# Performance work log

Hardware: AMD Instinct MI355X
Metric: run time of the kernel (lower is better)

The kernel has to match this reference:

```python
import jax, jax.numpy as jnp
import numpy as np

EMBED_DIM = 2048
NUM_HEADS = 16
HEAD_DIM = EMBED_DIM // NUM_HEADS
LATENT_DIM = 512


def setup_inputs() -> dict:
    key = jax.random.key(0)
    ks = jax.random.split(key, 6)
    s = 1.0 / np.sqrt(EMBED_DIM)
    sl = 1.0 / np.sqrt(LATENT_DIM)
    x = jax.random.normal(ks[0], (2, 2048, EMBED_DIM), dtype=jnp.float32)
    # nn.Linear stores weight as [out, in]; we keep [in, out] for x @ W
    W_q = jax.random.uniform(ks[1], (EMBED_DIM, EMBED_DIM), jnp.float32, -s, s)
    W_c = jax.random.uniform(ks[2], (EMBED_DIM, LATENT_DIM), jnp.float32, -s, s)
    W_k = jax.random.uniform(ks[3], (LATENT_DIM, EMBED_DIM), jnp.float32, -sl, sl)
    W_v = jax.random.uniform(ks[4], (LATENT_DIM, EMBED_DIM), jnp.float32, -sl, sl)
    W_o = jax.random.uniform(ks[5], (EMBED_DIM, EMBED_DIM), jnp.float32, -s, s)
    return {"x": x, "W_q": W_q, "W_c": W_c, "W_k": W_k, "W_v": W_v, "W_o": W_o}


def reference(x, W_q, W_c, W_k, W_v, W_o):
    B, S, _ = x.shape
    H, D = NUM_HEADS, HEAD_DIM
    Q = (x @ W_q).reshape(B, S, H, D)          # [B,S,H,D]
    C = x @ W_c                                 # [B,S,latent]
    K = (C @ W_k).reshape(B, S, H, D)
    V = (C @ W_v).reshape(B, S, H, D)
    scale = 1.0 / np.sqrt(D).astype(np.float32)
    scores = jnp.einsum('bqhd,bkhd->bhqk', Q, K) * scale
    probs = jax.nn.softmax(scores, axis=-1)
    attn = jnp.einsum('bhqk,bkhd->bqhd', probs, V).reshape(B, S, H * D)
    return attn @ W_o
```

## Files before the change

kernel.cpp:

```cpp
#include <hip/hip_runtime.h>
#include <hip/hip_bf16.h>
#include <cstdint>
#include <cstddef>

#define EDIM 2048
#define SLEN 2048
#define BATCH 2
#define NH 16
#define HD 128
#define LAT 512
#define MROWS (BATCH * SLEN)

#define QPREMUL (0.08838834764831845f * 1.44269504088896340f)

typedef __bf16 bf16;
typedef __bf16 bf16x8 __attribute__((ext_vector_type(8)));
typedef __bf16 bf16x4 __attribute__((ext_vector_type(4)));
typedef float f32x4 __attribute__((ext_vector_type(4)));
typedef float f32x16 __attribute__((ext_vector_type(16)));

#define AS1 __attribute__((address_space(1)))
#define AS3 __attribute__((address_space(3)))

__device__ __forceinline__ void gload_lds16(const void* g, void* l) {
  __builtin_amdgcn_global_load_lds((const AS1 void*)g, (AS3 void*)l, 16, 0, 0);
}

__global__ __launch_bounds__(256) void cvt_f32_bf16(const float* __restrict__ in,
                                                    bf16* __restrict__ out, int n4) {
  int i = blockIdx.x * blockDim.x + threadIdx.x;
  int stride = gridDim.x * blockDim.x;
  for (; i < n4; i += stride) {
    float4 v = reinterpret_cast<const float4*>(in)[i];
    bf16x4 o = {(bf16)v.x, (bf16)v.y, (bf16)v.z, (bf16)v.w};
    reinterpret_cast<bf16x4*>(out)[i] = o;
  }
}

__global__ __launch_bounds__(256) void transpose_cvt(const float* __restrict__ W,
                                                     bf16* __restrict__ Wt,
                                                     int K, int N) {
  __shared__ float tile[32][33];
  const int tx = threadIdx.x, ty = threadIdx.y;
  const int n0 = blockIdx.x * 32, k0 = blockIdx.y * 32;
#pragma unroll
  for (int i = 0; i < 4; ++i)
    tile[ty + i * 8][tx] = W[(size_t)(k0 + ty + i * 8) * N + n0 + tx];
  __syncthreads();
#pragma unroll
  for (int i = 0; i < 4; ++i)
    Wt[(size_t)(n0 + ty + i * 8) * K + k0 + tx] = (bf16)tile[tx][ty + i * 8];
}

enum { P_F32 = 0, P_QC = 1, P_FRAGKV = 2 };

#define BUFSZ 24576

#define STAGE_B_UNIT(dstbuf, k0)                                                 \
  {                                                                              \
    _Pragma("unroll") for (int jj = 0; jj < 2; ++jj) {                           \
      int L = t + jj * 512;                                                      \
      int row = L >> 3, c = L & 7;                                               \
      gload_lds16(Bt + (size_t)(n0 + row) * K + (k0) + ((c ^ (row & 7)) << 3),   \
                  (dstbuf) + 16384 + L * 8);                                     \
    }                                                                            \
  }

#define STAGE_A_PART(dstbuf, k0, jj)                                             \
  {                                                                              \
    int L = t256 + (jj) * 256;                                                   \
    int row = ahalf * 128 + (L >> 3), c = L & 7;                                 \
    gload_lds16(A + (size_t)(m0 + row) * K + (k0) + ((c ^ (row & 7)) << 3),      \
                (dstbuf) + row * 64 + c * 8);                                    \
  }

template <int MODE>
__global__ __launch_bounds__(512, 1)
void gemm8p(const bf16* __restrict__ A, const bf16* __restrict__ Bt,
            float* __restrict__ Cf, bf16* __restrict__ Cb, bf16* __restrict__ Cb2,
            int M, int N, int K) {
  extern __shared__ bf16 lds[];
  const int t = threadIdx.x;
  const int wid = t >> 6, l = t & 63, lo = l & 15, hi = l >> 4;
  const int wr = wid >> 1, wc = wid & 1;
  const int lin = blockIdx.y * gridDim.x + blockIdx.x;
  const int cpx = (gridDim.x * gridDim.y) >> 3;
  const int sw = (lin & 7) * cpx + (lin >> 3);
  const int m0 = (sw / gridDim.x) * 256, n0 = (sw % gridDim.x) * 128;
  const int nk = K >> 6;
  const int t256 = t & 255, ahalf = t >> 8;

  int aoff[2][4], boff[2][4];
#pragma unroll
  for (int kk = 0; kk < 2; ++kk)
#pragma unroll
    for (int m = 0; m < 4; ++m) {
      int ra = wr * 64 + m * 16 + lo;
      aoff[kk][m] = ra * 64 + (((kk * 4 + hi) ^ (ra & 7)) << 3);
      int rb = wc * 64 + m * 16 + lo;
      boff[kk][m] = 16384 + rb * 64 + (((kk * 4 + hi) ^ (rb & 7)) << 3);
    }

  f32x4 acc[4][4] = {};

  {
    bf16* b0 = lds;
    STAGE_B_UNIT(b0, 0);
    STAGE_A_PART(b0, 0, 0); STAGE_A_PART(b0, 0, 1);
    STAGE_A_PART(b0, 0, 2); STAGE_A_PART(b0, 0, 3);
    if (nk > 1) {
      bf16* b1 = lds + BUFSZ;
      STAGE_B_UNIT(b1, 64);
      STAGE_A_PART(b1, 64, 0); STAGE_A_PART(b1, 64, 1);
      STAGE_A_PART(b1, 64, 2); STAGE_A_PART(b1, 64, 3);
      asm volatile("s_waitcnt vmcnt(6)" ::: "memory");
    } else {
      asm volatile("s_waitcnt vmcnt(0)" ::: "memory");
    }
    __builtin_amdgcn_s_barrier();
  }

  int bsel = 0;
  for (int tt = 0; tt < nk; ++tt) {
    bf16* buf = lds + bsel * BUFSZ;
    bf16* nb = lds + ((bsel + 2) % 3) * BUFSZ;
    const bool pre = (tt + 2) < nk;
    const int k2 = (tt + 2) << 6;
    bf16x8 af[4], bfr[4];

#pragma unroll
    for (int m = 0; m < 4; ++m) af[m] = *reinterpret_cast<const bf16x8*>(buf + aoff[0][m]);
#pragma unroll
    for (int n = 0; n < 4; ++n) bfr[n] = *reinterpret_cast<const bf16x8*>(buf + boff[0][n]);
    if (pre) {
      STAGE_B_UNIT(nb, k2);
      STAGE_A_PART(nb, k2, 0); STAGE_A_PART(nb, k2, 1);
    }
    __builtin_amdgcn_s_barrier();
    asm volatile("s_waitcnt lgkmcnt(0)" ::: "memory");
    __builtin_amdgcn_s_setprio(1);
#pragma unroll
    for (int m = 0; m < 4; ++m)
#pragma unroll
      for (int n = 0; n < 4; ++n)
        acc[m][n] = __builtin_amdgcn_mfma_f32_16x16x32_bf16(af[m], bfr[n], acc[m][n], 0, 0, 0);
    __builtin_amdgcn_s_setprio(0);
    __builtin_amdgcn_s_barrier();

#pragma unroll
    for (int m = 0; m < 4; ++m) af[m] = *reinterpret_cast<const bf16x8*>(buf + aoff[1][m]);
#pragma unroll
    for (int n = 0; n < 4; ++n) bfr[n] = *reinterpret_cast<const bf16x8*>(buf + boff[1][n]);
    if (pre) { STAGE_A_PART(nb, k2, 2); STAGE_A_PART(nb, k2, 3); }
    __builtin_amdgcn_s_barrier();
    asm volatile("s_waitcnt lgkmcnt(0)" ::: "memory");
    __builtin_amdgcn_s_setprio(1);
#pragma unroll
    for (int m = 0; m < 4; ++m)
#pragma unroll
      for (int n = 0; n < 4; ++n)
        acc[m][n] = __builtin_amdgcn_mfma_f32_16x16x32_bf16(af[m], bfr[n], acc[m][n], 0, 0, 0);
    __builtin_amdgcn_s_setprio(0);
    if (tt < nk - 2) {
      asm volatile("s_waitcnt vmcnt(6)" ::: "memory");
    } else if (tt == nk - 2) {
      asm volatile("s_waitcnt vmcnt(0)" ::: "memory");
    }
    __builtin_amdgcn_s_barrier();
    bsel = (bsel == 2) ? 0 : bsel + 1;
  }

#pragma unroll
  for (int m = 0; m < 4; ++m) {
    const int rowb = m0 + wr * 64 + m * 16 + hi * 4;
#pragma unroll
    for (int n = 0; n < 4; ++n) {
      const int col = n0 + wc * 64 + n * 16 + lo;
      f32x4 v = acc[m][n];
#pragma unroll
      for (int r = 0; r < 4; ++r) {
        const int row = rowb + r;
        if constexpr (MODE == P_F32) {
          Cf[(size_t)row * N + col] = v[r];
        } else if constexpr (MODE == P_QC) {
          int bb = row >> 11, s = row & 2047;
          if (col < EDIM) {
            int h = col >> 7, dd = col & 127;
            size_t addr = (((size_t)(bb * NH + h) * 64 + (s >> 5)) << 12) +
                          ((dd >> 3) << 8) + ((s & 31) << 3) + (dd & 7);
            Cb[addr] = (bf16)(v[r] * QPREMUL);
          } else {
            Cb2[(size_t)row * LAT + (col - EDIM)] = (bf16)v[r];
          }
        } else {
          int bb = row >> 11, s = row & 2047;
          if (col < EDIM) {
            int h = col >> 7, dd = col & 127;
            size_t addr = (((size_t)(bb * NH + h) * 32 + (s >> 6)) << 14) +
                          (((s >> 5) & 1) << 12) + ((dd >> 3) << 8) +
                          ((s & 31) << 3) + (dd & 7);
            Cb[addr] = (bf16)v[r];
          } else {
            int c2 = col - EDIM;
            int h = c2 >> 7, d7 = c2 & 127;
            size_t addr = (((size_t)(bb * NH + h) * 32 + (s >> 6)) << 14) + 8192 +
                          ((d7 >> 5) << 11) + (((s & 63) >> 3) << 8) +
                          ((d7 & 31) << 3) + (s & 7);
            Cb[addr] = (bf16)v[r];
          }
        }
      }
    }
  }
}

__global__ __launch_bounds__(256) void attn_fwd32(const bf16* __restrict__ Qf,
                                                  const bf16* __restrict__ KVf,
                                                  bf16* __restrict__ O) {
  __shared__ bf16 sbuf[2][16384];
  const int t = threadIdx.x, w = t >> 6, l = t & 63;
  const int q = l & 31, hi1 = l >> 5;
  const int wg = blockIdx.y * 16 + blockIdx.x;
  const int wgs = (wg & 7) * 32 + (wg >> 3);
  const int qt = wgs & 15, h = wgs >> 4;
  const int b = blockIdx.z;
  const int bh = b * NH + h;
  const size_t kvbase = (size_t)bh * (32 * 16384);
  const size_t qbase = ((size_t)bh * 64 + qt * 4 + w) * 4096;

  bf16x8 qf[8];
#pragma unroll
  for (int ks = 0; ks < 8; ++ks)
    qf[ks] = *reinterpret_cast<const bf16x8*>(Qf + qbase + ks * 512 + l * 8);

#pragma unroll
  for (int i = 0; i < 8; ++i) {
    int c = i * 256 + t;
    gload_lds16(KVf + kvbase + c * 8, &sbuf[0][c * 8]);
  }
  __syncthreads();

  f32x16 ot[4] = {};
  float lsum = 0.f;
  int cur = 0;

  for (int kt = 0; kt < 32; ++kt) {
    if (kt + 1 < 32) {
      const bf16* src = KVf + kvbase + (size_t)(kt + 1) * 16384;
      bf16* dst = sbuf[cur ^ 1];
#pragma unroll
      for (int i = 0; i < 8; ++i) {
        int c = i * 256 + t;
        gload_lds16(src + c * 8, dst + c * 8);
      }
    }
    const bf16* sK = sbuf[cur];
    const bf16* sV = sbuf[cur] + 8192;

    f32x16 st[2] = {};
    __builtin_amdgcn_s_setprio(1);
#pragma unroll
    for (int kb = 0; kb < 2; ++kb)
#pragma unroll
      for (int ks = 0; ks < 8; ++ks) {
        bf16x8 kf = *reinterpret_cast<const bf16x8*>(sK + kb * 4096 + ks * 512 + l * 8);
        st[kb] = __builtin_amdgcn_mfma_f32_32x32x16_bf16(kf, qf[ks], st[kb], 0, 0, 0);
      }
    __builtin_amdgcn_s_setprio(0);

    float ts = 0.f;
#pragma unroll
    for (int kb = 0; kb < 2; ++kb)
#pragma unroll
      for (int r = 0; r < 16; ++r) {
        float e = __builtin_amdgcn_exp2f(st[kb][r]);
        st[kb][r] = e;
        ts += e;
      }
    lsum += ts;

    bf16x8 pa[4];
#pragma unroll
    for (int kb = 0; kb < 2; ++kb)
#pragma unroll
      for (int fh = 0; fh < 2; ++fh) {
        union W2 { bf16 h2[2]; unsigned u; };
        W2 a, bw, cw, dw;
        a.h2[0] = (bf16)st[kb][8 * fh + 0]; a.h2[1] = (bf16)st[kb][8 * fh + 1];
        bw.h2[0] = (bf16)st[kb][8 * fh + 4]; bw.h2[1] = (bf16)st[kb][8 * fh + 5];
        cw.h2[0] = (bf16)st[kb][8 * fh + 2]; cw.h2[1] = (bf16)st[kb][8 * fh + 3];
        dw.h2[0] = (bf16)st[kb][8 * fh + 6]; dw.h2[1] = (bf16)st[kb][8 * fh + 7];
        unsigned sAB = hi1 ? a.u : bw.u;
        unsigned gAB = __shfl_xor(sAB, 32);
        unsigned w0 = hi1 ? gAB : a.u;
        unsigned w2 = hi1 ? bw.u : gAB;
        unsigned sCD = hi1 ? cw.u : dw.u;
        unsigned gCD = __shfl_xor(sCD, 32);
        unsigned w1 = hi1 ? gCD : cw.u;
        unsigned w3 = hi1 ? dw.u : gCD;
        union FW { unsigned wd[4]; bf16x8 v; } fw;
        fw.wd[0] = w0; fw.wd[1] = w1; fw.wd[2] = w2; fw.wd[3] = w3;
        pa[kb * 2 + fh] = fw.v;
      }

    __builtin_amdgcn_s_setprio(1);
#pragma unroll
    for (int db = 0; db < 4; ++db)
#pragma unroll
      for (int ks = 0; ks < 4; ++ks) {
        bf16x8 vf = *reinterpret_cast<const bf16x8*>(sV + db * 2048 + ks * 512 + l * 8);
        ot[db] = __builtin_amdgcn_mfma_f32_32x32x16_bf16(vf, pa[ks], ot[db], 0, 0, 0);
      }
    __builtin_amdgcn_s_setprio(0);

    __syncthreads();
    cur ^= 1;
  }

  const float linv = 1.0f / (lsum + __shfl_xor(lsum, 32));
  const size_t orow = ((size_t)b * SLEN + qt * 128 + w * 32 + q) * EDIM + h * HD;
#pragma unroll
  for (int db = 0; db < 4; ++db)
#pragma unroll
    for (int g = 0; g < 4; ++g) {
      bf16x4 ov = {(bf16)(ot[db][4 * g + 0] * linv), (bf16)(ot[db][4 * g + 1] * linv),
                   (bf16)(ot[db][4 * g + 2] * linv), (bf16)(ot[db][4 * g + 3] * linv)};
      *reinterpret_cast<bf16x4*>(&O[orow + db * 32 + 8 * g + 4 * hi1]) = ov;
    }
}

extern "C" void kernel_launch(void* const* d_in, const int* in_sizes, int n_in,
                              void* d_out, int out_size, void* d_ws, size_t ws_size,
                              hipStream_t stream) {
  const float* x  = (const float*)d_in[0];
  const float* Wq = (const float*)d_in[1];
  const float* Wc = (const float*)d_in[2];
  const float* Wk = (const float*)d_in[3];
  const float* Wv = (const float*)d_in[4];
  const float* Wo = (const float*)d_in[5];
  float* out = (float*)d_out;

  char* ws = (char*)d_ws;
  size_t off = 0;
  auto alloc = [&](size_t bytes) {
    void* p = ws + off;
    off += (bytes + 255) & ~(size_t)255;
    return p;
  };
  bf16* XB   = (bf16*)alloc((size_t)MROWS * EDIM * 2);
  bf16* WQCT = (bf16*)alloc((size_t)(EDIM + LAT) * EDIM * 2);
  bf16* WKVT = (bf16*)alloc((size_t)2 * EDIM * LAT * 2);
  bf16* WOT  = (bf16*)alloc((size_t)EDIM * EDIM * 2);
  bf16* Qfr  = (bf16*)alloc((size_t)MROWS * EDIM * 2);
  bf16* Cm   = (bf16*)alloc((size_t)MROWS * LAT * 2);
  bf16* KVf  = (bf16*)alloc((size_t)2 * MROWS * EDIM * 2);
  bf16* Am   = (bf16*)alloc((size_t)MROWS * EDIM * 2);
  (void)ws_size; (void)in_sizes; (void)n_in; (void)out_size;

  const int LDSB = BUFSZ * 3 * 2;
  hipFuncSetAttribute((const void*)&gemm8p<P_QC>,     hipFuncAttributeMaxDynamicSharedMemorySize, LDSB);
  hipFuncSetAttribute((const void*)&gemm8p<P_FRAGKV>, hipFuncAttributeMaxDynamicSharedMemorySize, LDSB);
  hipFuncSetAttribute((const void*)&gemm8p<P_F32>,    hipFuncAttributeMaxDynamicSharedMemorySize, LDSB);

  dim3 tb(32, 8);
  cvt_f32_bf16<<<4096, 256, 0, stream>>>(x, XB, MROWS * EDIM / 4);
  transpose_cvt<<<dim3(EDIM / 32, EDIM / 32), tb, 0, stream>>>(Wq, WQCT, EDIM, EDIM);
  transpose_cvt<<<dim3(LAT / 32, EDIM / 32), tb, 0, stream>>>(Wc, WQCT + (size_t)EDIM * EDIM, EDIM, LAT);
  transpose_cvt<<<dim3(EDIM / 32, LAT / 32), tb, 0, stream>>>(Wk, WKVT, LAT, EDIM);
  transpose_cvt<<<dim3(EDIM / 32, LAT / 32), tb, 0, stream>>>(Wv, WKVT + (size_t)EDIM * LAT, LAT, EDIM);
  transpose_cvt<<<dim3(EDIM / 32, EDIM / 32), tb, 0, stream>>>(Wo, WOT, EDIM, EDIM);

  gemm8p<P_QC><<<dim3((EDIM + LAT) / 128, MROWS / 256), 512, LDSB, stream>>>(
      XB, WQCT, nullptr, Qfr, Cm, MROWS, EDIM + LAT, EDIM);
  gemm8p<P_FRAGKV><<<dim3(2 * EDIM / 128, MROWS / 256), 512, LDSB, stream>>>(
      Cm, WKVT, nullptr, KVf, nullptr, MROWS, 2 * EDIM, LAT);

  attn_fwd32<<<dim3(SLEN / 128, NH, BATCH), 256, 0, stream>>>(Qfr, KVf, Am);

  gemm8p<P_F32><<<dim3(EDIM / 128, MROWS / 256), 512, LDSB, stream>>>(
      Am, WOT, out, nullptr, nullptr, MROWS, EDIM, EDIM);
}
```

Baseline: 253.8 us.

## Software-pipeline attention loop with 4-stage half-tile LDS ring and QK/PV overlap

```diff
diff --git a/kernel.cpp b/kernel.cpp
--- a/kernel.cpp
+++ b/kernel.cpp
@@ -214,10 +214,80 @@
   }
 }
 
+#define ATT_STAGE(st_)                                                            \
+  {                                                                               \
+    const int T_ = (st_) >> 1, hh_ = (st_) & 1;                                   \
+    bf16* d_ = sbuf[(st_) & 3];                                                   \
+    const bf16* s_ = KV + T_ * 16384;                                             \
+    _Pragma("unroll") for (int ii = 0; ii < 2; ++ii) {                            \
+      int c_ = t + ii * 256;                                                      \
+      gload_lds16(s_ + hh_ * 4096 + c_ * 8, d_ + c_ * 8);                         \
+      int db_ = c_ >> 7, cw_ = c_ & 127;                                          \
+      gload_lds16(s_ + 8192 + db_ * 2048 + hh_ * 1024 + cw_ * 8,                  \
+                  d_ + 4096 + c_ * 8);                                            \
+    }                                                                             \
+  }
+
+#define ATT_QK(st_, sb_)                                                          \
+  {                                                                               \
+    const bf16* sk_ = (sb_);                                                      \
+    st_ = f32x16{};                                                               \
+    __builtin_amdgcn_s_setprio(1);                                                \
+    _Pragma("unroll") for (int ks = 0; ks < 8; ++ks) {                            \
+      bf16x8 kf = *reinterpret_cast<const bf16x8*>(sk_ + ks * 512 + l * 8);       \
+      st_ = __builtin_amdgcn_mfma_f32_32x32x16_bf16(kf, qf[ks], st_, 0, 0, 0);    \
+    }                                                                             \
+    __builtin_amdgcn_s_setprio(0);                                                \
+  }
+
+#define ATT_SMPACK(st_, pa_)                                                      \
+  {                                                                               \
+    float ts_ = 0.f;                                                              \
+    _Pragma("unroll") for (int r = 0; r < 16; ++r) {                              \
+      float e_ = __builtin_amdgcn_exp2f(st_[r]);                                  \
+      st_[r] = e_;                                                                \
+      ts_ += e_;                                                                  \
+    }                                                                             \
+    lsum += ts_;                                                                  \
+    _Pragma("unroll") for (int fh = 0; fh < 2; ++fh) {                            \
+      union W2 { bf16 h2[2]; unsigned u; };                                       \
+      W2 a_, b_, c_, d2_;                                                         \
+      a_.h2[0] = (bf16)st_[8 * fh + 0]; a_.h2[1] = (bf16)st_[8 * fh + 1];         \
+      b_.h2[0] = (bf16)st_[8 * fh + 4]; b_.h2[1] = (bf16)st_[8 * fh + 5];         \
+      c_.h2[0] = (bf16)st_[8 * fh + 2]; c_.h2[1] = (bf16)st_[8 * fh + 3];         \
+      d2_.h2[0] = (bf16)st_[8 * fh + 6]; d2_.h2[1] = (bf16)st_[8 * fh + 7];       \
+      unsigned sAB = hi1 ? a_.u : b_.u;                                           \
+      unsigned gAB = __shfl_xor(sAB, 32);                                         \
+      unsigned w0 = hi1 ? gAB : a_.u;                                             \
+      unsigned w2 = hi1 ? b_.u : gAB;                                             \
+      unsigned sCD = hi1 ? c_.u : d2_.u;                                          \
+      unsigned gCD = __shfl_xor(sCD, 32);                                         \
+      unsigned w1 = hi1 ? gCD : c_.u;                                             \
+      unsigned w3 = hi1 ? d2_.u : gCD;                                            \
+      union FW { unsigned wd[4]; bf16x8 v; } fw;                                  \
+      fw.wd[0] = w0; fw.wd[1] = w1; fw.wd[2] = w2; fw.wd[3] = w3;                 \
+      pa_[fh] = fw.v;                                                             \
+    }                                                                             \
+  }
+
+#define ATT_PV(pa_, sb_)                                                          \
+  {                                                                               \
+    const bf16* sv_ = (sb_) + 4096;                                               \
+    __builtin_amdgcn_s_setprio(1);                                                \
+    _Pragma("unroll") for (int db = 0; db < 4; ++db)                              \
+      _Pragma("unroll") for (int ksl = 0; ksl < 2; ++ksl) {                       \
+        bf16x8 vf = *reinterpret_cast<const bf16x8*>(sv_ + db * 1024 +            \
+                                                     ksl * 512 + l * 8);          \
+        ot[db] = __builtin_amdgcn_mfma_f32_32x32x16_bf16(vf, pa_[ksl], ot[db],    \
+                                                         0, 0, 0);                \
+      }                                                                           \
+    __builtin_amdgcn_s_setprio(0);                                                \
+  }
+
 __global__ __launch_bounds__(256) void attn_fwd32(const bf16* __restrict__ Qf,
                                                   const bf16* __restrict__ KVf,
                                                   bf16* __restrict__ O) {
-  __shared__ bf16 sbuf[2][16384];
+  __shared__ bf16 sbuf[4][8192];
   const int t = threadIdx.x, w = t >> 6, l = t & 63;
   const int q = l & 31, hi1 = l >> 5;
   const int wg = blockIdx.y * 16 + blockIdx.x;
@@ -225,97 +295,49 @@
   const int qt = wgs & 15, h = wgs >> 4;
   const int b = blockIdx.z;
   const int bh = b * NH + h;
-  const size_t kvbase = (size_t)bh * (32 * 16384);
+  const bf16* KV = KVf + (size_t)bh * (32 * 16384);
   const size_t qbase = ((size_t)bh * 64 + qt * 4 + w) * 4096;
 
   bf16x8 qf[8];
 #pragma unroll
   for (int ks = 0; ks < 8; ++ks)
     qf[ks] = *reinterpret_cast<const bf16x8*>(Qf + qbase + ks * 512 + l * 8);
-
-#pragma unroll
-  for (int i = 0; i < 8; ++i) {
-    int c = i * 256 + t;
-    gload_lds16(KVf + kvbase + c * 8, &sbuf[0][c * 8]);
-  }
-  __syncthreads();
+  asm volatile("s_waitcnt vmcnt(0)" ::: "memory");
 
   f32x16 ot[4] = {};
   float lsum = 0.f;
-  int cur = 0;
-
-  for (int kt = 0; kt < 32; ++kt) {
-    if (kt + 1 < 32) {
-      const bf16* src = KVf + kvbase + (size_t)(kt + 1) * 16384;
-      bf16* dst = sbuf[cur ^ 1];
-#pragma unroll
-      for (int i = 0; i < 8; ++i) {
-        int c = i * 256 + t;
-        gload_lds16(src + c * 8, dst + c * 8);
-      }
-    }
-    const bf16* sK = sbuf[cur];
-    const bf16* sV = sbuf[cur] + 8192;
-
-    f32x16 st[2] = {};
-    __builtin_amdgcn_s_setprio(1);
-#pragma unroll
-    for (int kb = 0; kb < 2; ++kb)
-#pragma unroll
-      for (int ks = 0; ks < 8; ++ks) {
-        bf16x8 kf = *reinterpret_cast<const bf16x8*>(sK + kb * 4096 + ks * 512 + l * 8);
-        st[kb] = __builtin_amdgcn_mfma_f32_32x32x16_bf16(kf, qf[ks], st[kb], 0, 0, 0);
-      }
-    __builtin_amdgcn_s_setprio(0);
-
-    float ts = 0.f;
-#pragma unroll
-    for (int kb = 0; kb < 2; ++kb)
-#pragma unroll
-      for (int r = 0; r < 16; ++r) {
-        float e = __builtin_amdgcn_exp2f(st[kb][r]);
-        st[kb][r] = e;
-        ts += e;
-      }
-    lsum += ts;
-
-    bf16x8 pa[4];
-#pragma unroll
-    for (int kb = 0; kb < 2; ++kb)
-#pragma unroll
-      for (int fh = 0; fh < 2; ++fh) {
-        union W2 { bf16 h2[2]; unsigned u; };
-        W2 a, bw, cw, dw;
-        a.h2[0] = (bf16)st[kb][8 * fh + 0]; a.h2[1] = (bf16)st[kb][8 * fh + 1];
-        bw.h2[0] = (bf16)st[kb][8 * fh + 4]; bw.h2[1] = (bf16)st[kb][8 * fh + 5];
-        cw.h2[0] = (bf16)st[kb][8 * fh + 2]; cw.h2[1] = (bf16)st[kb][8 * fh + 3];
-        dw.h2[0] = (bf16)st[kb][8 * fh + 6]; dw.h2[1] = (bf16)st[kb][8 * fh + 7];
-        unsigned sAB = hi1 ? a.u : bw.u;
-        unsigned gAB = __shfl_xor(sAB, 32);
-        unsigned w0 = hi1 ? gAB : a.u;
-        unsigned w2 = hi1 ? bw.u : gAB;
-        unsigned sCD = hi1 ? cw.u : dw.u;
-        unsigned gCD = __shfl_xor(sCD, 32);
-        unsigned w1 = hi1 ? gCD : cw.u;
-        unsigned w3 = hi1 ? dw.u : gCD;
-        union FW { unsigned wd[4]; bf16x8 v; } fw;
-        fw.wd[0] = w0; fw.wd[1] = w1; fw.wd[2] = w2; fw.wd[3] = w3;
-        pa[kb * 2 + fh] = fw.v;
-      }
-
-    __builtin_amdgcn_s_setprio(1);
-#pragma unroll
-    for (int db = 0; db < 4; ++db)
-#pragma unroll
-      for (int ks = 0; ks < 4; ++ks) {
-        bf16x8 vf = *reinterpret_cast<const bf16x8*>(sV + db * 2048 + ks * 512 + l * 8);
-        ot[db] = __builtin_amdgcn_mfma_f32_32x32x16_bf16(vf, pa[ks], ot[db], 0, 0, 0);
-      }
-    __builtin_amdgcn_s_setprio(0);
-
-    __syncthreads();
-    cur ^= 1;
-  }
+  f32x16 stA, stB;
+  bf16x8 paA[2], paB[2];
+
+  ATT_STAGE(0);
+  ATT_STAGE(1);
+  asm volatile("s_waitcnt vmcnt(4)" ::: "memory");
+  __builtin_amdgcn_s_barrier();
+  ATT_QK(stA, sbuf[0]);
+  ATT_STAGE(2);
+
+  for (int tt = 1; tt < 63; tt += 2) {
+    asm volatile("s_waitcnt vmcnt(4)" ::: "memory");
+    __builtin_amdgcn_s_barrier();
+    ATT_QK(stB, sbuf[tt & 3]);
+    ATT_SMPACK(stA, paA);
+    ATT_STAGE(tt + 2);
+    ATT_PV(paA, sbuf[(tt - 1) & 3]);
+    asm volatile("s_waitcnt vmcnt(4)" ::: "memory");
+    __builtin_amdgcn_s_barrier();
+    ATT_QK(stA, sbuf[(tt + 1) & 3]);
+    ATT_SMPACK(stB, paB);
+    if (tt + 3 < 64) ATT_STAGE(tt + 3);
+    ATT_PV(paB, sbuf[tt & 3]);
+  }
+
+  asm volatile("s_waitcnt vmcnt(0)" ::: "memory");
+  __builtin_amdgcn_s_barrier();
+  ATT_QK(stB, sbuf[3]);
+  ATT_SMPACK(stA, paA);
+  ATT_PV(paA, sbuf[2]);
+  ATT_SMPACK(stB, paB);
+  ATT_PV(paB, sbuf[3]);
 
   const float linv = 1.0f / (lsum + __shfl_xor(lsum, 32));
   const size_t orow = ((size_t)b * SLEN + qt * 128 + w * 32 + q) * EDIM + h * HD;
```

Result: no change. 250.7 us (-1.2%).
